# Performance work log

Hardware: AMD Instinct MI355X
Metric: run time of the kernel (lower is better)

## Reference

```python
import jax, jax.numpy as jnp
import numpy as np

BETA = 0.01  # soft-threshold level (init kwarg)
EPS = 1e-12


def vector_to_toeplitz(v):
    # v: [2N-1] complex generator; T[i, j] = v[N-1 + i - j], shape [N, N]
    n = (v.shape[0] + 1) // 2
    ii = jnp.arange(n)[:, None]
    jj = jnp.arange(n)[None, :]
    return v[(n - 1) + ii - jj]


def soft_thresh(z, beta):
    # complex soft-threshold (proximal op of beta*||.||_1):
    # z * max(|z| - beta, 0) / |z|
    mag = jnp.abs(z)
    scale = jnp.maximum(mag - beta, 0.0) / jnp.maximum(mag, EPS)
    return z * scale.astype(z.real.dtype)


def setup_inputs() -> dict:
    key = jax.random.key(0)
    ks = jax.random.split(key, 8)
    N, M, B = 1024, 256, 1024
    d = jnp.float32
    return {
        "v_re": jax.random.normal(ks[0], (2 * N - 1,), d),
        "v_im": jax.random.normal(ks[1], (2 * N - 1,), d),
        "W2_re": jax.random.normal(ks[2], (N, M), d) / np.sqrt(M),
        "W2_im": jax.random.normal(ks[3], (N, M), d) / np.sqrt(M),
        "x_re": jax.random.normal(ks[4], (N, B), d),
        "x_im": jax.random.normal(ks[5], (N, B), d),
        "y_re": jax.random.normal(ks[6], (M, B), d),
        "y_im": jax.random.normal(ks[7], (M, B), d),
    }


def reference(v_re, v_im, W2_re, W2_im, x_re, x_im, y_re, y_im):
    v = jax.lax.complex(v_re, v_im)      # [2N-1]
    W2 = jax.lax.complex(W2_re, W2_im)   # [N, M] (= A^H)
    x = jax.lax.complex(x_re, x_im)      # [N, B]
    y = jax.lax.complex(y_re, y_im)      # [M, B]
    W1 = vector_to_toeplitz(v)           # [N, N] Toeplitz
    # tpm(W1, x) + W2 @ y, then complex soft-threshold
    z = soft_thresh(W1 @ x + W2 @ y, BETA)  # [N, B]
    return z
```

## Files before the change

### kernel.cpp

```cpp
#include <hip/hip_runtime.h>
#include <hip/hip_fp16.h>
#include <cstdint>
#include <cstddef>


#define K_DIM 2560
#define BETA_F 0.01f
#define EPS_F  1e-12f

typedef __attribute__((ext_vector_type(8))) _Float16 half8;
typedef __attribute__((ext_vector_type(4))) _Float16 half4;
typedef __attribute__((ext_vector_type(4))) float   floatx4;

__device__ alignas(16) _Float16 g_Ap[1024 * K_DIM];
__device__ alignas(16) _Float16 g_Bt[2048 * K_DIM];

__global__ __launch_bounds__(256) void build_A(
    const float* __restrict__ v_re, const float* __restrict__ v_im,
    const float* __restrict__ W2_re, const float* __restrict__ W2_im)
{
    int t = blockIdx.x * 256 + threadIdx.x;
    int i  = t / 320;
    int c  = t - i * 320;
    int kp = c * 8;
    half8 h;
    if (kp < 1024) {
#pragma unroll
        for (int j = 0; j < 8; ++j) h[j] = (_Float16)v_re[1023 + i - kp - j];
    } else if (kp < 1280) {
        const float* s = W2_re + i * 256 + (kp - 1024);
#pragma unroll
        for (int j = 0; j < 8; ++j) h[j] = (_Float16)s[j];
    } else if (kp < 2304) {
        int k2 = kp - 1280;
#pragma unroll
        for (int j = 0; j < 8; ++j) h[j] = (_Float16)v_im[1023 + i - k2 - j];
    } else {
        const float* s = W2_im + i * 256 + (kp - 2304);
#pragma unroll
        for (int j = 0; j < 8; ++j) h[j] = (_Float16)s[j];
    }
    *reinterpret_cast<half8*>(g_Ap + (size_t)i * K_DIM + kp) = h;
}

__global__ __launch_bounds__(256) void build_Bt(
    const float* __restrict__ src_re, const float* __restrict__ src_im,
    int koff)
{
    __shared__ float lre[32][33];
    __shared__ float lim[32][33];
    int tid = threadIdx.x;
    int tx = tid & 31, ty = tid >> 5;
    int k0 = blockIdx.x * 32;
    int n0 = blockIdx.y * 32;
#pragma unroll
    for (int s = 0; s < 4; ++s) {
        int kk = ty + 8 * s;
        lre[kk][tx] = src_re[(size_t)(k0 + kk) * 1024 + n0 + tx];
        lim[kk][tx] = src_im[(size_t)(k0 + kk) * 1024 + n0 + tx];
    }
    __syncthreads();
    int lane_n = tid >> 3;
    int kq     = (tid & 7) * 4;
    half4 hre, him, hmim;
#pragma unroll
    for (int j = 0; j < 4; ++j) {
        float re = lre[kq + j][lane_n];
        float im = lim[kq + j][lane_n];
        hre[j]  = (_Float16)re;
        him[j]  = (_Float16)im;
        hmim[j] = (_Float16)(-im);
    }
    int n = n0 + lane_n;
    size_t kk2 = (size_t)koff + k0 + kq;
    _Float16* r0 = g_Bt + (size_t)(2 * n)     * K_DIM;
    _Float16* r1 = g_Bt + (size_t)(2 * n + 1) * K_DIM;
    *reinterpret_cast<half4*>(r0 + kk2)        = hre;
    *reinterpret_cast<half4*>(r0 + kk2 + 1280) = hmim;
    *reinterpret_cast<half4*>(r1 + kk2)        = him;
    *reinterpret_cast<half4*>(r1 + kk2 + 1280) = hre;
}

__global__ __launch_bounds__(256) void gemm_fused(float* __restrict__ out,
                                                  int out_n)
{
    __shared__ __align__(16) _Float16 As[2 * 64 * 32];
    __shared__ __align__(16) _Float16 Bs[2 * 64 * 32];

    const int tid  = threadIdx.x;
    const int lane = tid & 63;
    const int w    = tid >> 6;
    const int wm   = w >> 1;
    const int wn   = w & 1;

    const int bid = blockIdx.x;
    const int xcd = bid & 7;
    const int t   = bid >> 3;
    const int mi0 = ((xcd & 1) * 8 + (t & 7)) * 64;
    const int ni0 = ((xcd >> 1) * 8 + (t >> 3)) * 64;

    floatx4 acc[2][2];
#pragma unroll
    for (int a = 0; a < 2; ++a)
#pragma unroll
        for (int b = 0; b < 2; ++b) acc[a][b] = (floatx4)0.0f;

    const int rS = tid >> 2;
    const int jS = tid & 3;
    const int s0 = ((rS & 15) >> 1) & 3;
    char* asW = (char*)As + rS * 64 + ((jS ^ s0) * 16);
    char* bsW = (char*)Bs + rS * 64 + ((jS ^ s0) * 16);
    const _Float16* gA = g_Ap + (size_t)(mi0 + rS) * K_DIM + jS * 8;
    const _Float16* gB = g_Bt + (size_t)(ni0 + rS) * K_DIM + jS * 8;

    const int rowA = lane & 15;
    const int q    = lane >> 4;
    const int coff = (q ^ ((rowA >> 1) & 3)) * 16;

    half8 pA0 = *reinterpret_cast<const half8*>(gA);
    half8 pA1 = *reinterpret_cast<const half8*>(gA + 32);
    half8 pB0 = *reinterpret_cast<const half8*>(gB);
    half8 pB1 = *reinterpret_cast<const half8*>(gB + 32);

    for (int kt = 0; kt < K_DIM / 64; ++kt) {
        *reinterpret_cast<half8*>(asW)        = pA0;
        *reinterpret_cast<half8*>(asW + 4096) = pA1;
        *reinterpret_cast<half8*>(bsW)        = pB0;
        *reinterpret_cast<half8*>(bsW + 4096) = pB1;
        __syncthreads();
        if (kt < K_DIM / 64 - 1) {
            const _Float16* ga = gA + (kt + 1) * 64;
            const _Float16* gb = gB + (kt + 1) * 64;
            pA0 = *reinterpret_cast<const half8*>(ga);
            pA1 = *reinterpret_cast<const half8*>(ga + 32);
            pB0 = *reinterpret_cast<const half8*>(gb);
            pB1 = *reinterpret_cast<const half8*>(gb + 32);
        }
        half8 af[2][2], bf[2][2];
#pragma unroll
        for (int mi = 0; mi < 2; ++mi) {
            int r = wm * 32 + mi * 16 + rowA;
            af[mi][0] = *reinterpret_cast<const half8*>((char*)As + r * 64 + coff);
            af[mi][1] = *reinterpret_cast<const half8*>((char*)As + 4096 + r * 64 + coff);
        }
#pragma unroll
        for (int ni = 0; ni < 2; ++ni) {
            int r = wn * 32 + ni * 16 + rowA;
            bf[ni][0] = *reinterpret_cast<const half8*>((char*)Bs + r * 64 + coff);
            bf[ni][1] = *reinterpret_cast<const half8*>((char*)Bs + 4096 + r * 64 + coff);
        }
#pragma unroll
        for (int mi = 0; mi < 2; ++mi)
#pragma unroll
            for (int ni = 0; ni < 2; ++ni) {
                acc[mi][ni] = __builtin_amdgcn_mfma_f32_16x16x32_f16(
                    af[mi][0], bf[ni][0], acc[mi][ni], 0, 0, 0);
                acc[mi][ni] = __builtin_amdgcn_mfma_f32_16x16x32_f16(
                    af[mi][1], bf[ni][1], acc[mi][ni], 0, 0, 0);
            }
        __syncthreads();
    }

    const int colL  = lane & 15;
    const int rquad = (lane >> 4) * 4;
#pragma unroll
    for (int mi = 0; mi < 2; ++mi)
#pragma unroll
        for (int ni = 0; ni < 2; ++ni)
#pragma unroll
            for (int r = 0; r < 4; ++r) {
                float c = acc[mi][ni][r];
                float p = __shfl_xor(c, 1, 64);
                float mag = sqrtf(c * c + p * p);
                float s = fmaxf(mag - BETA_F, 0.0f) / fmaxf(mag, EPS_F);
                int row = mi0 + wm * 32 + mi * 16 + rquad + r;
                int col = ni0 + wn * 32 + ni * 16 + colL;
                if ((col & 1) == 0) {
                    size_t idx = (size_t)row * 1024 + (col >> 1);
                    if (idx < (size_t)out_n) out[idx] = c * s;
                }
            }
}

extern "C" void kernel_launch(void* const* d_in, const int* in_sizes, int n_in,
                              void* d_out, int out_size, void* d_ws, size_t ws_size,
                              hipStream_t stream) {
    (void)d_ws; (void)ws_size; (void)in_sizes; (void)n_in;
    const float* v_re  = (const float*)d_in[0];
    const float* v_im  = (const float*)d_in[1];
    const float* W2_re = (const float*)d_in[2];
    const float* W2_im = (const float*)d_in[3];
    const float* x_re  = (const float*)d_in[4];
    const float* x_im  = (const float*)d_in[5];
    const float* y_re  = (const float*)d_in[6];
    const float* y_im  = (const float*)d_in[7];
    float* out = (float*)d_out;

    build_A<<<1280, 256, 0, stream>>>(v_re, v_im, W2_re, W2_im);
    build_Bt<<<dim3(32, 32), 256, 0, stream>>>(x_re, x_im, 0);
    build_Bt<<<dim3(8, 32),  256, 0, stream>>>(y_re, y_im, 1024);
    gemm_fused<<<512, 256, 0, stream>>>(out, out_size);
}
```

Baseline: 117.3 us.

## Split-K GEMM with double-buffered LDS and separate reduce+soft-threshold kernel

```diff
diff --git a/kernel.cpp b/kernel.cpp
--- a/kernel.cpp
+++ b/kernel.cpp
@@ -14,6 +14,8 @@
 
 __device__ alignas(16) _Float16 g_Ap[1024 * K_DIM];
 __device__ alignas(16) _Float16 g_Bt[2048 * K_DIM];
+__device__ alignas(16) float    g_P0[1024 * 2048];
+__device__ alignas(16) float    g_P1[1024 * 2048];
 
 __global__ __launch_bounds__(256) void build_A(
     const float* __restrict__ v_re, const float* __restrict__ v_im,
@@ -44,20 +46,25 @@
 }
 
 __global__ __launch_bounds__(256) void build_Bt(
-    const float* __restrict__ src_re, const float* __restrict__ src_im,
-    int koff)
+    const float* __restrict__ x_re, const float* __restrict__ x_im,
+    const float* __restrict__ y_re, const float* __restrict__ y_im)
 {
     __shared__ float lre[32][33];
     __shared__ float lim[32][33];
     int tid = threadIdx.x;
     int tx = tid & 31, ty = tid >> 5;
-    int k0 = blockIdx.x * 32;
+    int bx = blockIdx.x;
+    const float* sre = (bx < 32) ? x_re : y_re;
+    const float* sim = (bx < 32) ? x_im : y_im;
+    int kb   = (bx < 32) ? bx : (bx - 32);
+    int koff = (bx < 32) ? 0 : 1024;
+    int k0 = kb * 32;
     int n0 = blockIdx.y * 32;
 #pragma unroll
     for (int s = 0; s < 4; ++s) {
         int kk = ty + 8 * s;
-        lre[kk][tx] = src_re[(size_t)(k0 + kk) * 1024 + n0 + tx];
-        lim[kk][tx] = src_im[(size_t)(k0 + kk) * 1024 + n0 + tx];
+        lre[kk][tx] = sre[(size_t)(k0 + kk) * 1024 + n0 + tx];
+        lim[kk][tx] = sim[(size_t)(k0 + kk) * 1024 + n0 + tx];
     }
     __syncthreads();
     int lane_n = tid >> 3;
@@ -81,11 +88,10 @@
     *reinterpret_cast<half4*>(r1 + kk2 + 1280) = hre;
 }
 
-__global__ __launch_bounds__(256) void gemm_fused(float* __restrict__ out,
-                                                  int out_n)
-{
-    __shared__ __align__(16) _Float16 As[2 * 64 * 32];
-    __shared__ __align__(16) _Float16 Bs[2 * 64 * 32];
+__global__ __launch_bounds__(256) void gemm_split(void)
+{
+    __shared__ __align__(16) _Float16 As[2 * 2 * 64 * 32];
+    __shared__ __align__(16) _Float16 Bs[2 * 2 * 64 * 32];
 
     const int tid  = threadIdx.x;
     const int lane = tid & 63;
@@ -93,11 +99,15 @@
     const int wm   = w >> 1;
     const int wn   = w & 1;
 
-    const int bid = blockIdx.x;
-    const int xcd = bid & 7;
-    const int t   = bid >> 3;
+    const int bid   = blockIdx.x;
+    const int split = bid >> 9;
+    const int sb    = bid & 511;
+    const int xcd   = sb & 7;
+    const int t     = sb >> 3;
     const int mi0 = ((xcd & 1) * 8 + (t & 7)) * 64;
     const int ni0 = ((xcd >> 1) * 8 + (t >> 3)) * 64;
+    const int ks  = split * 1280;
+    float* __restrict__ P = split ? g_P1 : g_P0;
 
     floatx4 acc[2][2];
 #pragma unroll
@@ -110,25 +120,30 @@
     const int s0 = ((rS & 15) >> 1) & 3;
     char* asW = (char*)As + rS * 64 + ((jS ^ s0) * 16);
     char* bsW = (char*)Bs + rS * 64 + ((jS ^ s0) * 16);
-    const _Float16* gA = g_Ap + (size_t)(mi0 + rS) * K_DIM + jS * 8;
-    const _Float16* gB = g_Bt + (size_t)(ni0 + rS) * K_DIM + jS * 8;
+    const _Float16* gA = g_Ap + (size_t)(mi0 + rS) * K_DIM + ks + jS * 8;
+    const _Float16* gB = g_Bt + (size_t)(ni0 + rS) * K_DIM + ks + jS * 8;
 
     const int rowA = lane & 15;
     const int q    = lane >> 4;
     const int coff = (q ^ ((rowA >> 1) & 3)) * 16;
 
-    half8 pA0 = *reinterpret_cast<const half8*>(gA);
-    half8 pA1 = *reinterpret_cast<const half8*>(gA + 32);
-    half8 pB0 = *reinterpret_cast<const half8*>(gB);
-    half8 pB1 = *reinterpret_cast<const half8*>(gB + 32);
-
-    for (int kt = 0; kt < K_DIM / 64; ++kt) {
+    {
+        half8 pA0 = *reinterpret_cast<const half8*>(gA);
+        half8 pA1 = *reinterpret_cast<const half8*>(gA + 32);
+        half8 pB0 = *reinterpret_cast<const half8*>(gB);
+        half8 pB1 = *reinterpret_cast<const half8*>(gB + 32);
         *reinterpret_cast<half8*>(asW)        = pA0;
         *reinterpret_cast<half8*>(asW + 4096) = pA1;
         *reinterpret_cast<half8*>(bsW)        = pB0;
         *reinterpret_cast<half8*>(bsW + 4096) = pB1;
-        __syncthreads();
-        if (kt < K_DIM / 64 - 1) {
+    }
+    __syncthreads();
+
+    const int NIT = 1280 / 64;
+    for (int kt = 0; kt < NIT; ++kt) {
+        const int cur = kt & 1;
+        half8 pA0, pA1, pB0, pB1;
+        if (kt < NIT - 1) {
             const _Float16* ga = gA + (kt + 1) * 64;
             const _Float16* gb = gB + (kt + 1) * 64;
             pA0 = *reinterpret_cast<const half8*>(ga);
@@ -136,18 +151,20 @@
             pB0 = *reinterpret_cast<const half8*>(gb);
             pB1 = *reinterpret_cast<const half8*>(gb + 32);
         }
+        const char* Ab = (const char*)As + cur * 8192;
+        const char* Bb = (const char*)Bs + cur * 8192;
         half8 af[2][2], bf[2][2];
 #pragma unroll
         for (int mi = 0; mi < 2; ++mi) {
             int r = wm * 32 + mi * 16 + rowA;
-            af[mi][0] = *reinterpret_cast<const half8*>((char*)As + r * 64 + coff);
-            af[mi][1] = *reinterpret_cast<const half8*>((char*)As + 4096 + r * 64 + coff);
+            af[mi][0] = *reinterpret_cast<const half8*>(Ab + r * 64 + coff);
+            af[mi][1] = *reinterpret_cast<const half8*>(Ab + 4096 + r * 64 + coff);
         }
 #pragma unroll
         for (int ni = 0; ni < 2; ++ni) {
             int r = wn * 32 + ni * 16 + rowA;
-            bf[ni][0] = *reinterpret_cast<const half8*>((char*)Bs + r * 64 + coff);
-            bf[ni][1] = *reinterpret_cast<const half8*>((char*)Bs + 4096 + r * 64 + coff);
+            bf[ni][0] = *reinterpret_cast<const half8*>(Bb + r * 64 + coff);
+            bf[ni][1] = *reinterpret_cast<const half8*>(Bb + 4096 + r * 64 + coff);
         }
 #pragma unroll
         for (int mi = 0; mi < 2; ++mi)
@@ -158,6 +175,14 @@
                 acc[mi][ni] = __builtin_amdgcn_mfma_f32_16x16x32_f16(
                     af[mi][1], bf[ni][1], acc[mi][ni], 0, 0, 0);
             }
+        if (kt < NIT - 1) {
+            char* aw = asW + (cur ^ 1) * 8192;
+            char* bw = bsW + (cur ^ 1) * 8192;
+            *reinterpret_cast<half8*>(aw)        = pA0;
+            *reinterpret_cast<half8*>(aw + 4096) = pA1;
+            *reinterpret_cast<half8*>(bw)        = pB0;
+            *reinterpret_cast<half8*>(bw + 4096) = pB1;
+        }
         __syncthreads();
     }
 
@@ -169,17 +194,28 @@
         for (int ni = 0; ni < 2; ++ni)
 #pragma unroll
             for (int r = 0; r < 4; ++r) {
-                float c = acc[mi][ni][r];
-                float p = __shfl_xor(c, 1, 64);
-                float mag = sqrtf(c * c + p * p);
-                float s = fmaxf(mag - BETA_F, 0.0f) / fmaxf(mag, EPS_F);
                 int row = mi0 + wm * 32 + mi * 16 + rquad + r;
                 int col = ni0 + wn * 32 + ni * 16 + colL;
-                if ((col & 1) == 0) {
-                    size_t idx = (size_t)row * 1024 + (col >> 1);
-                    if (idx < (size_t)out_n) out[idx] = c * s;
-                }
+                P[(size_t)row * 2048 + col] = acc[mi][ni][r];
             }
+}
+
+__global__ __launch_bounds__(256) void reduce_soft(float* __restrict__ out,
+                                                   int out_n)
+{
+    int t = blockIdx.x * 256 + threadIdx.x;
+    floatx4 v0 = reinterpret_cast<const floatx4*>(g_P0)[t];
+    floatx4 v1 = reinterpret_cast<const floatx4*>(g_P1)[t];
+    float re0 = v0[0] + v1[0], im0 = v0[1] + v1[1];
+    float re1 = v0[2] + v1[2], im1 = v0[3] + v1[3];
+    float m0 = sqrtf(re0 * re0 + im0 * im0);
+    float m1 = sqrtf(re1 * re1 + im1 * im1);
+    float s0 = fmaxf(m0 - BETA_F, 0.0f) / fmaxf(m0, EPS_F);
+    float s1 = fmaxf(m1 - BETA_F, 0.0f) / fmaxf(m1, EPS_F);
+    float2 r = make_float2(re0 * s0, re1 * s1);
+    int idx = t * 2;
+    if (idx + 1 < out_n)
+        *reinterpret_cast<float2*>(out + idx) = r;
 }
 
 extern "C" void kernel_launch(void* const* d_in, const int* in_sizes, int n_in,
@@ -197,7 +233,7 @@
     float* out = (float*)d_out;
 
     build_A<<<1280, 256, 0, stream>>>(v_re, v_im, W2_re, W2_im);
-    build_Bt<<<dim3(32, 32), 256, 0, stream>>>(x_re, x_im, 0);
-    build_Bt<<<dim3(8, 32),  256, 0, stream>>>(y_re, y_im, 1024);
-    gemm_fused<<<512, 256, 0, stream>>>(out, out_size);
-}
+    build_Bt<<<dim3(40, 32), 256, 0, stream>>>(x_re, x_im, y_re, y_im);
+    gemm_split<<<1024, 256, 0, stream>>>();
+    reduce_soft<<<2048, 256, 0, stream>>>(out, out_size);
+}
```

New measurement: 116.9 us. About the same (-0.3%).
